# Kernel tuning notes

Measured on AMD Instinct MI355X. Metric: run time of the kernel, lower is better.

The kernel has to match this reference:

```python
import jax, jax.numpy as jnp
import numpy as np

N_NODES = 100000
N_EDGES = 800000


def gcn_conv(x, W, b, src, dst, ew, n):
    # PyG GCNConv with edge weights and self-loops already included in (src, dst, ew):
    # deg[i] = sum of incoming edge weights at i; norm_e = d^-1/2[src] * w_e * d^-1/2[dst]
    h = x @ W                                                  # [N, F_out]
    deg = jax.ops.segment_sum(ew, dst, num_segments=n)         # [N]
    dinv = jnp.where(deg > 0, jax.lax.rsqrt(deg), 0.0)
    norm = dinv[src] * ew * dinv[dst]                          # [E]
    out = jax.ops.segment_sum(h[src] * norm[:, None], dst, num_segments=n)
    return out + b


def add_self_loops(edge_index, edge_weight, n):
    loop = jnp.arange(n, dtype=edge_index.dtype)
    src = jnp.concatenate([edge_index[0], loop])
    dst = jnp.concatenate([edge_index[1], loop])
    ew = jnp.concatenate([edge_weight, jnp.ones((n,), edge_weight.dtype)])
    return src, dst, ew


def setup_inputs() -> dict:
    key = jax.random.key(0)
    ks = jax.random.split(key, 10)
    x = jax.random.normal(ks[0], (N_NODES, 5), jnp.float32)
    edge_index = jax.random.randint(ks[1], (2, N_EDGES), 0, N_NODES, dtype=jnp.int64)
    edge_weight = jax.random.uniform(ks[2], (N_EDGES,), jnp.float32)
    def glorot(k, fan_in, fan_out):
        s = float(np.sqrt(6.0 / (fan_in + fan_out)))
        return jax.random.uniform(k, (fan_in, fan_out), jnp.float32, -s, s)
    return {
        "x": x,
        "edge_index": edge_index,
        "edge_weight": edge_weight,
        "W1": glorot(ks[3], 5, 320),
        "b1": jnp.zeros((320,), jnp.float32),
        "W2": glorot(ks[4], 320, 160),
        "b2": jnp.zeros((160,), jnp.float32),
        "We": glorot(ks[5], 160, 80),
        "be": jnp.zeros((80,), jnp.float32),
    }


def reference(x, edge_index, edge_weight, W1, b1, W2, b2, We, be):
    n = x.shape[0]
    src, dst, ew = add_self_loops(edge_index, edge_weight, n)
    h = gcn_conv(x, W1, b1, src, dst, ew, n)        # conv1
    h = jax.nn.relu(h)
    h = gcn_conv(h, W2, b2, src, dst, ew, n)        # conv2
    return h @ We + be                              # embed linear
```

## Files before the change

kernel.cpp:

```cpp
#include <hip/hip_runtime.h>

#define NF0 5
#define F1 320
#define F2 160
#define F3 80
#define NSUB 8
#define SUBCAP 512

typedef float f32x4 __attribute__((ext_vector_type(4)));
typedef _Float16 f16x8 __attribute__((ext_vector_type(8)));


__global__ void k_prep(const float* __restrict__ x, float* __restrict__ xp, int N,
                       int padz, int* __restrict__ zreg, int zwords, int padxB,
                       const float* __restrict__ W2, const float* __restrict__ We,
                       _Float16* __restrict__ Bh,
                       const float* __restrict__ b2, const float* __restrict__ be,
                       float* __restrict__ bc,
                       const unsigned int* __restrict__ ei32, int E, int* __restrict__ flag) {
    __shared__ int ok;
    int b = blockIdx.x;
    if (b < padz) {
        int t = b * 256 + threadIdx.x;
        if (t < zwords) zreg[t] = 0;
        return;
    }
    b -= padz;
    if (b < padxB) {
        int t = b * 256 + threadIdx.x;
        if (t < N * 8) {
            int f = t & 7, i = t >> 3;
            xp[t] = (f < NF0) ? x[i * NF0 + f] : 0.f;
        }
    } else if (b < padxB + 13) {
        int t = (b - padxB) * 256 + threadIdx.x;
        if (t >= 50 * 64) return;
        int fid = t >> 6, lane = t & 63;
        int kk = fid / 5, ct = fid % 5;
        int col = ct * 16 + (lane & 15);
        int row0 = kk * 32 + (lane >> 4) * 8;
        float acc[8] = {0.f, 0.f, 0.f, 0.f, 0.f, 0.f, 0.f, 0.f};
        for (int m = 0; m < F2; ++m) {
            float wv = We[m * F3 + col];
            #pragma unroll
            for (int i = 0; i < 8; ++i)
                acc[i] += W2[(size_t)(row0 + i) * F2 + m] * wv;
        }
        size_t ob = (size_t)t * 8;
        #pragma unroll
        for (int i = 0; i < 8; ++i)
            Bh[ob + i] = (_Float16)acc[i];
    } else if (b == padxB + 13) {
        int j = threadIdx.x;
        if (j < F3) {
            float s = be[j];
            for (int k = 0; k < F2; ++k) s += b2[k] * We[k * F3 + j];
            bc[j] = s;
        }
    } else {
        if (threadIdx.x == 0) ok = 1;
        __syncthreads();
        int npairs = E < 2048 ? E : 2048;
        for (int i = threadIdx.x; i < npairs; i += blockDim.x)
            if (ei32[2 * i + 1] != 0u) ok = 0;
        __syncthreads();
        if (threadIdx.x == 0) *flag = ok;
    }
}


__global__ void k_binA(const void* ei, const float* __restrict__ ew, const int* __restrict__ flag,
                       int* __restrict__ bin_cnt , int2* __restrict__ bins,
                       int n_bins, int* __restrict__ ovf_n, int* __restrict__ ovf,
                       int ovf_cap, int E) {
    int e = blockIdx.x * blockDim.x + threadIdx.x;
    if (e >= E) return;
    int sub = blockIdx.x & (NSUB - 1);
    int s, d;
    if (*flag) {
        const long long* p = (const long long*)ei;
        s = (int)p[e]; d = (int)p[E + e];
    } else {
        const int* p = (const int*)ei;
        s = p[e]; d = p[E + e];
    }
    float w = ew[e];
    int b = d >> 8;
    int pos = atomicAdd(&bin_cnt[(sub * n_bins + b) * 4], 1);
    if (pos < SUBCAP) {
        int2 pk;
        pk.x = s | ((d & 255) << 24);
        pk.y = __float_as_int(w);
        bins[(size_t)b * (NSUB * SUBCAP) + sub * SUBCAP + pos] = pk;
    } else {
        int o = atomicAdd(ovf_n, 1);
        if (o < ovf_cap) {
            ovf[3 * o] = s; ovf[3 * o + 1] = d; ovf[3 * o + 2] = __float_as_int(w);
        }
    }
}


__global__ __launch_bounds__(256) void k_binB1(const int2* __restrict__ bins,
                                               const int* __restrict__ bin_cnt, int n_bins,
                                               float* __restrict__ dinv, float* __restrict__ xp,
                                               const int* __restrict__ ovf_n,
                                               const int* __restrict__ ovf, int ovf_cap, int N) {
    __shared__ float deg_l[256];
    int b = blockIdx.x, t = threadIdx.x;
    deg_l[t] = 0.f;
    __syncthreads();
    for (int sub = 0; sub < NSUB; ++sub) {
        int ne = bin_cnt[(sub * n_bins + b) * 4]; if (ne > SUBCAP) ne = SUBCAP;
        const int2* bp = bins + (size_t)b * (NSUB * SUBCAP) + sub * SUBCAP;
        for (int j = t; j < ne; j += 256) {
            int2 pk = bp[j];
            atomicAdd(&deg_l[((unsigned int)pk.x) >> 24], __int_as_float(pk.y));
        }
    }
    int n = *ovf_n; if (n > ovf_cap) n = ovf_cap;
    int lo = b * 256;
    for (int j = t; j < n; j += 256) {
        int d = ovf[3 * j + 1];
        if (d >= lo && d < lo + 256)
            atomicAdd(&deg_l[d - lo], __int_as_float(ovf[3 * j + 2]));
    }
    __syncthreads();
    int node = lo + t;
    if (node < N) {
        float di = rsqrtf(1.0f + deg_l[t]);
        dinv[node] = di;
        float4* xr = (float4*)(xp + (size_t)node * 8);
        float4 v0 = xr[0], v1 = xr[1];
        v0.x *= di; v0.y *= di; v0.z *= di; v0.w *= di;
        v1.x *= di; v1.y *= di; v1.z *= di; v1.w *= di;
        xr[0] = v0; xr[1] = v1;
    }
}


__global__ __launch_bounds__(256) void k_binB2(const int2* __restrict__ bins,
                                               const int* __restrict__ bin_cnt, int n_bins,
                                               const float* __restrict__ dinv,
                                               const float* __restrict__ xp,
                                               int* __restrict__ cnt, int2* __restrict__ bucket,
                                               int cap, float* __restrict__ agg1,
                                               int* __restrict__ ovf_n, int* __restrict__ ovf,
                                               int ovf_cap, int N) {
    __shared__ int cnt_l[256];
    __shared__ float acc_l[256 * NF0];
    int b = blockIdx.x, t = threadIdx.x;
    cnt_l[t] = 0;
    for (int q = t; q < 256 * NF0; q += 256) acc_l[q] = 0.f;
    int nsnap = *ovf_n; if (nsnap > ovf_cap) nsnap = ovf_cap;
    __syncthreads();
    int lo = b * 256;

    for (int j = t; j < nsnap; j += 256) {
        int d = ovf[3 * j + 1];
        if (d >= lo && d < lo + 256) {
            int s = ovf[3 * j];
            float w = __int_as_float(ovf[3 * j + 2]);
            float4 sv = *(const float4*)(xp + (size_t)s * 8);
            float s4 = xp[(size_t)s * 8 + 4];
            int dl = d - lo;
            atomicAdd(&acc_l[dl * NF0 + 0], sv.x * w);
            atomicAdd(&acc_l[dl * NF0 + 1], sv.y * w);
            atomicAdd(&acc_l[dl * NF0 + 2], sv.z * w);
            atomicAdd(&acc_l[dl * NF0 + 3], sv.w * w);
            atomicAdd(&acc_l[dl * NF0 + 4], s4 * w);
        }
    }

    for (int sub = 0; sub < NSUB; ++sub) {
        int ne = bin_cnt[(sub * n_bins + b) * 4]; if (ne > SUBCAP) ne = SUBCAP;
        const int2* bp = bins + (size_t)b * (NSUB * SUBCAP) + sub * SUBCAP;
        for (int j = t; j < ne; j += 256) {
            int2 pk = bp[j];
            int s = pk.x & 0xFFFFFF;
            int dl = ((unsigned int)pk.x) >> 24;
            float w = __int_as_float(pk.y);
            int node = lo + dl;
            int pos = atomicAdd(&cnt_l[dl], 1);
            if (pos < cap) {
                int2 out_pk; out_pk.x = s; out_pk.y = pk.y;
                bucket[(size_t)node * cap + pos] = out_pk;
            } else {
                int o = atomicAdd(ovf_n, 1);
                if (o < ovf_cap) { ovf[3 * o] = s; ovf[3 * o + 1] = node; ovf[3 * o + 2] = pk.y; }
            }
            float4 sv = *(const float4*)(xp + (size_t)s * 8);
            float s4 = xp[(size_t)s * 8 + 4];
            atomicAdd(&acc_l[dl * NF0 + 0], sv.x * w);
            atomicAdd(&acc_l[dl * NF0 + 1], sv.y * w);
            atomicAdd(&acc_l[dl * NF0 + 2], sv.z * w);
            atomicAdd(&acc_l[dl * NF0 + 3], sv.w * w);
            atomicAdd(&acc_l[dl * NF0 + 4], s4 * w);
        }
    }
    __syncthreads();

    int node = lo + t;
    if (node < N) {
        float di = dinv[node];
        float4 xv = *(const float4*)(xp + (size_t)node * 8);
        float x4 = xp[(size_t)node * 8 + 4];
        float* op = agg1 + (size_t)node * NF0;
        op[0] = di * (acc_l[t * NF0 + 0] + xv.x);
        op[1] = di * (acc_l[t * NF0 + 1] + xv.y);
        op[2] = di * (acc_l[t * NF0 + 2] + xv.z);
        op[3] = di * (acc_l[t * NF0 + 3] + xv.w);
        op[4] = di * (acc_l[t * NF0 + 4] + x4);
        int c = cnt_l[t]; if (c > cap) c = cap;
        cnt[node] = c;
    }
}


__global__ __launch_bounds__(256) void k_node(const float* __restrict__ agg1,
                                              const float* __restrict__ W1,
                                              const float* __restrict__ b1,
                                              const _Float16* __restrict__ Bh,
                                              const float* __restrict__ dinv,
                                              _Float16* __restrict__ g, int N) {
    __shared__ float W_l[6 * F1];
    int tid = threadIdx.x;
    for (int i = tid; i < 480; i += 256) {
        float4 v = (i < 400) ? ((const float4*)W1)[i] : ((const float4*)b1)[i - 400];
        ((float4*)W_l)[i] = v;
    }
    __syncthreads();

    int w = tid >> 6, l = tid & 63;
    int nl = l & 15, kg = l >> 4;
    int base = blockIdx.x * 64 + w * 16;
    int n0 = base + nl;

    float a0v[5] = {0.f, 0.f, 0.f, 0.f, 0.f};
    if (n0 < N) {
        const float* ap = agg1 + (size_t)n0 * NF0;
        #pragma unroll
        for (int j = 0; j < 5; ++j) a0v[j] = ap[j];
    }

    f32x4 zero = {0.f, 0.f, 0.f, 0.f};
    f32x4 acc[5] = {zero, zero, zero, zero, zero};
    const f16x8* bhp = (const f16x8*)Bh;

    #pragma unroll
    for (int kk = 0; kk < 10; ++kk) {
        int k0 = kk * 32 + kg * 8;
        float v0[8];
        const float* bb = W_l + 5 * F1 + k0;
        #pragma unroll
        for (int i = 0; i < 8; ++i) v0[i] = bb[i];
        #pragma unroll
        for (int j = 0; j < 5; ++j) {
            const float* wp = W_l + j * F1 + k0;
            float aj0 = a0v[j];
            #pragma unroll
            for (int i = 0; i < 8; ++i) v0[i] += aj0 * wp[i];
        }
        f16x8 ah0, al0;
        #pragma unroll
        for (int i = 0; i < 8; ++i) {
            float t0 = fmaxf(v0[i], 0.f);
            _Float16 h0 = (_Float16)t0;
            ah0[i] = h0;
            al0[i] = (_Float16)(t0 - (float)h0);
        }
        #pragma unroll
        for (int ct = 0; ct < 5; ++ct) {
            f16x8 bf = bhp[(kk * 5 + ct) * 64 + l];
            acc[ct] = __builtin_amdgcn_mfma_f32_16x16x32_f16(ah0, bf, acc[ct], 0, 0, 0);
            acc[ct] = __builtin_amdgcn_mfma_f32_16x16x32_f16(al0, bf, acc[ct], 0, 0, 0);
        }
    }

    #pragma unroll
    for (int r = 0; r < 4; ++r) {
        int r0 = base + kg * 4 + r;
        if (r0 < N) {
            float dv = dinv[r0];
            #pragma unroll
            for (int ct = 0; ct < 5; ++ct)
                g[(size_t)r0 * F3 + ct * 16 + nl] = (_Float16)(acc[ct][r] * dv);
        }
    }
}


__global__ __launch_bounds__(256) void k_aggB(const _Float16* __restrict__ g,
                                              const float* __restrict__ dinv,
                                              const float* __restrict__ bc,
                                              const int* __restrict__ cnt,
                                              const int2* __restrict__ bucket, int cap,
                                              float* __restrict__ out, int N) {
    int t = blockIdx.x * blockDim.x + threadIdx.x;
    if (t >= 5 * N) return;
    int i = t / 5;
    int c = (t - i * 5) << 4;
    float acc[16];
    #pragma unroll
    for (int e = 0; e < 16; ++e) acc[e] = 0.f;
    int cn = cnt[i];
    const int2* row = bucket + (size_t)i * cap;
    #pragma unroll 2
    for (int j = 0; j < cn; ++j) {
        int2 pk = row[j];
        float w = __int_as_float(pk.y);
        const f16x8* sp = (const f16x8*)(g + (size_t)pk.x * F3 + c);
        f16x8 a = sp[0], b8 = sp[1];
        #pragma unroll
        for (int e = 0; e < 8; ++e) {
            acc[e]     += (float)a[e]  * w;
            acc[8 + e] += (float)b8[e] * w;
        }
    }
    float di = dinv[i];
    const f16x8* sp = (const f16x8*)(g + (size_t)i * F3 + c);
    f16x8 u0 = sp[0], u1 = sp[1];
    const float4* bp = (const float4*)(bc + c);
    float4 q0 = bp[0], q1 = bp[1], q2 = bp[2], q3 = bp[3];
    float4 o0, o1, o2, o3;
    o0.x = di * (acc[0]  + (float)u0[0]) + q0.x;
    o0.y = di * (acc[1]  + (float)u0[1]) + q0.y;
    o0.z = di * (acc[2]  + (float)u0[2]) + q0.z;
    o0.w = di * (acc[3]  + (float)u0[3]) + q0.w;
    o1.x = di * (acc[4]  + (float)u0[4]) + q1.x;
    o1.y = di * (acc[5]  + (float)u0[5]) + q1.y;
    o1.z = di * (acc[6]  + (float)u0[6]) + q1.z;
    o1.w = di * (acc[7]  + (float)u0[7]) + q1.w;
    o2.x = di * (acc[8]  + (float)u1[0]) + q2.x;
    o2.y = di * (acc[9]  + (float)u1[1]) + q2.y;
    o2.z = di * (acc[10] + (float)u1[2]) + q2.z;
    o2.w = di * (acc[11] + (float)u1[3]) + q2.w;
    o3.x = di * (acc[12] + (float)u1[4]) + q3.x;
    o3.y = di * (acc[13] + (float)u1[5]) + q3.y;
    o3.z = di * (acc[14] + (float)u1[6]) + q3.z;
    o3.w = di * (acc[15] + (float)u1[7]) + q3.w;
    float4* op = (float4*)(out + (size_t)i * F3 + c);
    op[0] = o0; op[1] = o1; op[2] = o2; op[3] = o3;
}

__global__ void k_fixB(const _Float16* __restrict__ g, const float* __restrict__ dinv,
                       const int* __restrict__ ovf_n, const int* __restrict__ ovf, int ovf_cap,
                       float* __restrict__ out) {
    int n = *ovf_n; if (n > ovf_cap) n = ovf_cap;
    for (int j = blockIdx.x * blockDim.x + threadIdx.x; j < n; j += gridDim.x * blockDim.x) {
        int s = ovf[3 * j], d = ovf[3 * j + 1];
        float w = dinv[d] * __int_as_float(ovf[3 * j + 2]);
        for (int f = 0; f < F3; ++f)
            atomicAdd(&out[(size_t)d * F3 + f], (float)g[(size_t)s * F3 + f] * w);
    }
}


static inline size_t align256(size_t x) { return (x + 255) & ~(size_t)255; }

extern "C" void kernel_launch(void* const* d_in, const int* in_sizes, int n_in,
                              void* d_out, int out_size, void* d_ws, size_t ws_size,
                              hipStream_t stream) {
    const float* x  = (const float*)d_in[0];
    const void*  ei = d_in[1];
    const float* ew = (const float*)d_in[2];
    const float* W1 = (const float*)d_in[3];
    const float* b1 = (const float*)d_in[4];
    const float* W2 = (const float*)d_in[5];
    const float* b2 = (const float*)d_in[6];
    const float* We = (const float*)d_in[7];
    const float* be = (const float*)d_in[8];
    float* out = (float*)d_out;

    int N = in_sizes[0] / NF0;
    int E = in_sizes[2];

    const int OVF_CAP = 131072;
    int n_bins = (N + 255) >> 8;

    char* p = (char*)d_ws;
    auto alloc = [&](size_t bytes) { char* r = p; p += align256(bytes); return r; };
    int*   flag  = (int*)alloc(4);
    int zwords = 16 + NSUB * n_bins * 4;
    int*   zreg  = (int*)alloc((size_t)zwords * 4);
    int*   ovf_n = zreg;
    int*   bin_cnt = zreg + 16;
    float* dinv  = (float*)alloc((size_t)N * 4);
    int*   cnt   = (int*)  alloc((size_t)N * 4);
    int*   ovf   = (int*)  alloc((size_t)OVF_CAP * 12);
    int2*  bins  = (int2*) alloc((size_t)n_bins * NSUB * SUBCAP * 8);
    float* xp    = (float*)alloc((size_t)N * 8 * 4);
    float* agg1  = (float*)alloc((size_t)N * NF0 * 4);
    float* bc    = (float*)alloc((size_t)F3 * 4);
    _Float16* Bh = (_Float16*)alloc((size_t)50 * 64 * 8 * 2);
    _Float16* g  = (_Float16*)alloc((size_t)N * F3 * 2);

    size_t used = (size_t)(p - (char*)d_ws);
    int cap = 24;
    if (ws_size > used) {
        size_t avail = (ws_size - used) / ((size_t)N * 8);
        if (avail < (size_t)cap) cap = (int)avail;
    } else cap = 4;
    if (cap < 4) cap = 4;
    int2* bucket = (int2*)alloc((size_t)N * cap * 8);

    int eb    = (E + 255) / 256;
    int padz  = (zwords + 255) / 256;
    int padxB = (N * 8 + 255) / 256;

    k_prep<<<padz + padxB + 15, 256, 0, stream>>>(x, xp, N, padz, zreg, zwords, padxB,
                                                  W2, We, Bh, b2, be, bc,
                                                  (const unsigned int*)ei, E, flag);

    k_binA<<<eb, 256, 0, stream>>>(ei, ew, flag, bin_cnt, bins, n_bins, ovf_n, ovf, OVF_CAP, E);
    k_binB1<<<n_bins, 256, 0, stream>>>(bins, bin_cnt, n_bins, dinv, xp, ovf_n, ovf, OVF_CAP, N);
    k_binB2<<<n_bins, 256, 0, stream>>>(bins, bin_cnt, n_bins, dinv, xp, cnt, bucket, cap,
                                        agg1, ovf_n, ovf, OVF_CAP, N);

    k_node<<<(N + 63) / 64, 256, 0, stream>>>(agg1, W1, b1, Bh, dinv, g, N);
    k_aggB<<<(5 * N + 255) / 256, 256, 0, stream>>>(g, dinv, bc, cnt, bucket, cap, out, N);
    k_fixB<<<16, 256, 0, stream>>>(g, dinv, ovf_n, ovf, OVF_CAP, out);
}
```

Baseline: 182.5 us.

## Drop padded x copy, widen binning blocks, stage Bh in LDS, unroll aggregation

Removes the padded, dinv-prescaled copy of x. The source dinv is applied per edge inside binB2, and the self term uses dinv squared. The binning kernels use 512 threads so that two sub-bins are processed concurrently. k_node copies the fused W2·We fp16 matrix into shared memory, and the edge aggregation loop is manually unrolled by two for more loads in flight. This trades an extra dinv gather per edge and unaligned float4 loads of x for one fewer pass over memory.

```diff
diff --git a/kernel.cpp b/kernel.cpp
--- a/kernel.cpp
+++ b/kernel.cpp
@@ -11,8 +11,7 @@
 typedef _Float16 f16x8 __attribute__((ext_vector_type(8)));
 
 
-__global__ void k_prep(const float* __restrict__ x, float* __restrict__ xp, int N,
-                       int padz, int* __restrict__ zreg, int zwords, int padxB,
+__global__ void k_prep(int padz, int* __restrict__ zreg, int zwords,
                        const float* __restrict__ W2, const float* __restrict__ We,
                        _Float16* __restrict__ Bh,
                        const float* __restrict__ b2, const float* __restrict__ be,
@@ -26,14 +25,8 @@
         return;
     }
     b -= padz;
-    if (b < padxB) {
+    if (b < 13) {
         int t = b * 256 + threadIdx.x;
-        if (t < N * 8) {
-            int f = t & 7, i = t >> 3;
-            xp[t] = (f < NF0) ? x[i * NF0 + f] : 0.f;
-        }
-    } else if (b < padxB + 13) {
-        int t = (b - padxB) * 256 + threadIdx.x;
         if (t >= 50 * 64) return;
         int fid = t >> 6, lane = t & 63;
         int kk = fid / 5, ct = fid % 5;
@@ -50,7 +43,7 @@
         #pragma unroll
         for (int i = 0; i < 8; ++i)
             Bh[ob + i] = (_Float16)acc[i];
-    } else if (b == padxB + 13) {
+    } else if (b == 13) {
         int j = threadIdx.x;
         if (j < F3) {
             float s = be[j];
@@ -101,48 +94,43 @@
 }
 
 
-__global__ __launch_bounds__(256) void k_binB1(const int2* __restrict__ bins,
+__global__ __launch_bounds__(512) void k_binB1(const int2* __restrict__ bins,
                                                const int* __restrict__ bin_cnt, int n_bins,
-                                               float* __restrict__ dinv, float* __restrict__ xp,
+                                               float* __restrict__ dinv,
                                                const int* __restrict__ ovf_n,
                                                const int* __restrict__ ovf, int ovf_cap, int N) {
     __shared__ float deg_l[256];
     int b = blockIdx.x, t = threadIdx.x;
-    deg_l[t] = 0.f;
+    if (t < 256) deg_l[t] = 0.f;
     __syncthreads();
-    for (int sub = 0; sub < NSUB; ++sub) {
+    int th = t >> 8;
+    int tt = t & 255;
+    for (int sp = 0; sp < NSUB; sp += 2) {
+        int sub = sp + th;
         int ne = bin_cnt[(sub * n_bins + b) * 4]; if (ne > SUBCAP) ne = SUBCAP;
         const int2* bp = bins + (size_t)b * (NSUB * SUBCAP) + sub * SUBCAP;
-        for (int j = t; j < ne; j += 256) {
+        for (int j = tt; j < ne; j += 256) {
             int2 pk = bp[j];
             atomicAdd(&deg_l[((unsigned int)pk.x) >> 24], __int_as_float(pk.y));
         }
     }
     int n = *ovf_n; if (n > ovf_cap) n = ovf_cap;
     int lo = b * 256;
-    for (int j = t; j < n; j += 256) {
+    for (int j = t; j < n; j += 512) {
         int d = ovf[3 * j + 1];
         if (d >= lo && d < lo + 256)
             atomicAdd(&deg_l[d - lo], __int_as_float(ovf[3 * j + 2]));
     }
     __syncthreads();
     int node = lo + t;
-    if (node < N) {
-        float di = rsqrtf(1.0f + deg_l[t]);
-        dinv[node] = di;
-        float4* xr = (float4*)(xp + (size_t)node * 8);
-        float4 v0 = xr[0], v1 = xr[1];
-        v0.x *= di; v0.y *= di; v0.z *= di; v0.w *= di;
-        v1.x *= di; v1.y *= di; v1.z *= di; v1.w *= di;
-        xr[0] = v0; xr[1] = v1;
-    }
-}
-
-
-__global__ __launch_bounds__(256) void k_binB2(const int2* __restrict__ bins,
+    if (t < 256 && node < N) dinv[node] = rsqrtf(1.0f + deg_l[t]);
+}
+
+
+__global__ __launch_bounds__(512) void k_binB2(const int2* __restrict__ bins,
                                                const int* __restrict__ bin_cnt, int n_bins,
                                                const float* __restrict__ dinv,
-                                               const float* __restrict__ xp,
+                                               const float* __restrict__ x,
                                                int* __restrict__ cnt, int2* __restrict__ bucket,
                                                int cap, float* __restrict__ agg1,
                                                int* __restrict__ ovf_n, int* __restrict__ ovf,
@@ -150,36 +138,35 @@
     __shared__ int cnt_l[256];
     __shared__ float acc_l[256 * NF0];
     int b = blockIdx.x, t = threadIdx.x;
-    cnt_l[t] = 0;
-    for (int q = t; q < 256 * NF0; q += 256) acc_l[q] = 0.f;
+    if (t < 256) cnt_l[t] = 0;
+    for (int q = t; q < 256 * NF0; q += 512) acc_l[q] = 0.f;
     int nsnap = *ovf_n; if (nsnap > ovf_cap) nsnap = ovf_cap;
     __syncthreads();
     int lo = b * 256;
 
-    for (int j = t; j < nsnap; j += 256) {
+    for (int j = t; j < nsnap; j += 512) {
         int d = ovf[3 * j + 1];
         if (d >= lo && d < lo + 256) {
             int s = ovf[3 * j];
-            float w = __int_as_float(ovf[3 * j + 2]);
-            float4 sv = *(const float4*)(xp + (size_t)s * 8);
-            float s4 = xp[(size_t)s * 8 + 4];
+            float w = __int_as_float(ovf[3 * j + 2]) * dinv[s];
+            const float* xs = x + (size_t)s * NF0;
             int dl = d - lo;
-            atomicAdd(&acc_l[dl * NF0 + 0], sv.x * w);
-            atomicAdd(&acc_l[dl * NF0 + 1], sv.y * w);
-            atomicAdd(&acc_l[dl * NF0 + 2], sv.z * w);
-            atomicAdd(&acc_l[dl * NF0 + 3], sv.w * w);
-            atomicAdd(&acc_l[dl * NF0 + 4], s4 * w);
-        }
-    }
-
-    for (int sub = 0; sub < NSUB; ++sub) {
+            #pragma unroll
+            for (int f = 0; f < NF0; ++f)
+                atomicAdd(&acc_l[dl * NF0 + f], xs[f] * w);
+        }
+    }
+
+    int th = t >> 8;
+    int tt = t & 255;
+    for (int sp = 0; sp < NSUB; sp += 2) {
+        int sub = sp + th;
         int ne = bin_cnt[(sub * n_bins + b) * 4]; if (ne > SUBCAP) ne = SUBCAP;
         const int2* bp = bins + (size_t)b * (NSUB * SUBCAP) + sub * SUBCAP;
-        for (int j = t; j < ne; j += 256) {
+        for (int j = tt; j < ne; j += 256) {
             int2 pk = bp[j];
             int s = pk.x & 0xFFFFFF;
             int dl = ((unsigned int)pk.x) >> 24;
-            float w = __int_as_float(pk.y);
             int node = lo + dl;
             int pos = atomicAdd(&cnt_l[dl], 1);
             if (pos < cap) {
@@ -189,8 +176,10 @@
                 int o = atomicAdd(ovf_n, 1);
                 if (o < ovf_cap) { ovf[3 * o] = s; ovf[3 * o + 1] = node; ovf[3 * o + 2] = pk.y; }
             }
-            float4 sv = *(const float4*)(xp + (size_t)s * 8);
-            float s4 = xp[(size_t)s * 8 + 4];
+            float w = __int_as_float(pk.y) * dinv[s];
+            const float* xs = x + (size_t)s * NF0;
+            float4 sv = *(const float4*)xs;
+            float s4 = xs[4];
             atomicAdd(&acc_l[dl * NF0 + 0], sv.x * w);
             atomicAdd(&acc_l[dl * NF0 + 1], sv.y * w);
             atomicAdd(&acc_l[dl * NF0 + 2], sv.z * w);
@@ -201,16 +190,14 @@
     __syncthreads();
 
     int node = lo + t;
-    if (node < N) {
+    if (t < 256 && node < N) {
         float di = dinv[node];
-        float4 xv = *(const float4*)(xp + (size_t)node * 8);
-        float x4 = xp[(size_t)node * 8 + 4];
+        float sc = di * di;
+        const float* xn = x + (size_t)node * NF0;
         float* op = agg1 + (size_t)node * NF0;
-        op[0] = di * (acc_l[t * NF0 + 0] + xv.x);
-        op[1] = di * (acc_l[t * NF0 + 1] + xv.y);
-        op[2] = di * (acc_l[t * NF0 + 2] + xv.z);
-        op[3] = di * (acc_l[t * NF0 + 3] + xv.w);
-        op[4] = di * (acc_l[t * NF0 + 4] + x4);
+        #pragma unroll
+        for (int f = 0; f < NF0; ++f)
+            op[f] = di * acc_l[t * NF0 + f] + sc * xn[f];
         int c = cnt_l[t]; if (c > cap) c = cap;
         cnt[node] = c;
     }
@@ -224,11 +211,17 @@
                                               const float* __restrict__ dinv,
                                               _Float16* __restrict__ g, int N) {
     __shared__ float W_l[6 * F1];
+    __shared__ _Float16 B_l[50 * 64 * 8];
     int tid = threadIdx.x;
     for (int i = tid; i < 480; i += 256) {
         float4 v = (i < 400) ? ((const float4*)W1)[i] : ((const float4*)b1)[i - 400];
         ((float4*)W_l)[i] = v;
     }
+    {
+        const float4* src = (const float4*)Bh;
+        float4* dst = (float4*)B_l;
+        for (int i = tid; i < 3200; i += 256) dst[i] = src[i];
+    }
     __syncthreads();
 
     int w = tid >> 6, l = tid & 63;
@@ -245,7 +238,7 @@
 
     f32x4 zero = {0.f, 0.f, 0.f, 0.f};
     f32x4 acc[5] = {zero, zero, zero, zero, zero};
-    const f16x8* bhp = (const f16x8*)Bh;
+    const f16x8* blp = (const f16x8*)B_l;
 
     #pragma unroll
     for (int kk = 0; kk < 10; ++kk) {
@@ -271,7 +264,7 @@
         }
         #pragma unroll
         for (int ct = 0; ct < 5; ++ct) {
-            f16x8 bf = bhp[(kk * 5 + ct) * 64 + l];
+            f16x8 bf = blp[(kk * 5 + ct) * 64 + l];
             acc[ct] = __builtin_amdgcn_mfma_f32_16x16x32_f16(ah0, bf, acc[ct], 0, 0, 0);
             acc[ct] = __builtin_amdgcn_mfma_f32_16x16x32_f16(al0, bf, acc[ct], 0, 0, 0);
         }
@@ -305,16 +298,30 @@
     for (int e = 0; e < 16; ++e) acc[e] = 0.f;
     int cn = cnt[i];
     const int2* row = bucket + (size_t)i * cap;
-    #pragma unroll 2
-    for (int j = 0; j < cn; ++j) {
-        int2 pk = row[j];
-        float w = __int_as_float(pk.y);
-        const f16x8* sp = (const f16x8*)(g + (size_t)pk.x * F3 + c);
-        f16x8 a = sp[0], b8 = sp[1];
+    int j = 0;
+    for (; j + 2 <= cn; j += 2) {
+        int2 p0 = row[j], p1 = row[j + 1];
+        float w0 = __int_as_float(p0.y);
+        float w1 = __int_as_float(p1.y);
+        const f16x8* s0 = (const f16x8*)(g + (size_t)p0.x * F3 + c);
+        const f16x8* s1 = (const f16x8*)(g + (size_t)p1.x * F3 + c);
+        f16x8 a0 = s0[0], b0 = s0[1];
+        f16x8 a1 = s1[0], b1 = s1[1];
         #pragma unroll
         for (int e = 0; e < 8; ++e) {
-            acc[e]     += (float)a[e]  * w;
-            acc[8 + e] += (float)b8[e] * w;
+            acc[e]     += (float)a0[e] * w0 + (float)a1[e] * w1;
+            acc[8 + e] += (float)b0[e] * w0 + (float)b1[e] * w1;
+        }
+    }
+    if (j < cn) {
+        int2 p0 = row[j];
+        float w0 = __int_as_float(p0.y);
+        const f16x8* s0 = (const f16x8*)(g + (size_t)p0.x * F3 + c);
+        f16x8 a0 = s0[0], b0 = s0[1];
+        #pragma unroll
+        for (int e = 0; e < 8; ++e) {
+            acc[e]     += (float)a0[e] * w0;
+            acc[8 + e] += (float)b0[e] * w0;
         }
     }
     float di = dinv[i];
@@ -389,7 +396,6 @@
     int*   cnt   = (int*)  alloc((size_t)N * 4);
     int*   ovf   = (int*)  alloc((size_t)OVF_CAP * 12);
     int2*  bins  = (int2*) alloc((size_t)n_bins * NSUB * SUBCAP * 8);
-    float* xp    = (float*)alloc((size_t)N * 8 * 4);
     float* agg1  = (float*)alloc((size_t)N * NF0 * 4);
     float* bc    = (float*)alloc((size_t)F3 * 4);
     _Float16* Bh = (_Float16*)alloc((size_t)50 * 64 * 8 * 2);
@@ -404,17 +410,15 @@
     if (cap < 4) cap = 4;
     int2* bucket = (int2*)alloc((size_t)N * cap * 8);
 
-    int eb    = (E + 255) / 256;
-    int padz  = (zwords + 255) / 256;
-    int padxB = (N * 8 + 255) / 256;
-
-    k_prep<<<padz + padxB + 15, 256, 0, stream>>>(x, xp, N, padz, zreg, zwords, padxB,
-                                                  W2, We, Bh, b2, be, bc,
-                                                  (const unsigned int*)ei, E, flag);
+    int eb   = (E + 255) / 256;
+    int padz = (zwords + 255) / 256;
+
+    k_prep<<<padz + 15, 256, 0, stream>>>(padz, zreg, zwords, W2, We, Bh, b2, be, bc,
+                                          (const unsigned int*)ei, E, flag);
 
     k_binA<<<eb, 256, 0, stream>>>(ei, ew, flag, bin_cnt, bins, n_bins, ovf_n, ovf, OVF_CAP, E);
-    k_binB1<<<n_bins, 256, 0, stream>>>(bins, bin_cnt, n_bins, dinv, xp, ovf_n, ovf, OVF_CAP, N);
-    k_binB2<<<n_bins, 256, 0, stream>>>(bins, bin_cnt, n_bins, dinv, xp, cnt, bucket, cap,
+    k_binB1<<<n_bins, 512, 0, stream>>>(bins, bin_cnt, n_bins, dinv, ovf_n, ovf, OVF_CAP, N);
+    k_binB2<<<n_bins, 512, 0, stream>>>(bins, bin_cnt, n_bins, dinv, x, cnt, bucket, cap,
                                         agg1, ovf_n, ovf, OVF_CAP, N);
 
     k_node<<<(N + 63) / 64, 256, 0, stream>>>(agg1, W1, b1, Bh, dinv, g, N);
```

After: 187.2 us. +2.5%, slower.
